# Optimization experiments

Measured on AMD Instinct MI355X. Metric: run time of the kernel, lower is better.

The kernel has to match this reference:

```python
import jax, jax.numpy as jnp
import numpy as np

B, H, W = 32, 256, 256
K = 8          # nonzero voting centers per image
NPIX = 6       # corner pixels per center
MARGIN = 10.0
RATIO_INV = 1e4
LW = {'center': 1.0, 'corner': 1.0, 'corner_offset': 0.25, 'corner_bin_offset': 1.0}


def setup_inputs() -> dict:
    rng = np.random.default_rng(0)
    out0 = rng.standard_normal((B, 7, H, W)).astype(np.float32)
    out1 = rng.standard_normal((B, 7, H, W)).astype(np.float32)
    t_corner = np.zeros((B, 1, H, W), np.float32)
    t_corner_offset = np.zeros((B, 1, 2, H, W), np.float32)
    t_bin = rng.uniform(-0.5, 0.5, (B, 1, 2, H, W)).astype(np.float32)
    anchors = np.zeros((B, K + 1), np.int32)
    positives = np.zeros((B, K + 1), np.int32)
    neg_zero = np.zeros((B, K + 1), np.int32)
    neg_other = np.zeros((B, K), np.int32)
    for b in range(B):
        flat = rng.choice(H * W, size=K * NPIX, replace=False)
        ys, xs = flat // W, flat % W
        t_corner[b, 0, ys, xs] = 1.0
        cvals = rng.choice(np.arange(1, 1000), K, replace=False).astype(np.float32)
        for k in range(K):
            s = slice(k * NPIX, (k + 1) * NPIX)
            v = cvals[k] - (ys[s] + xs[s]).astype(np.float32)
            t_corner_offset[b, 0, 0, ys[s], xs[s]] = 0.5 * v
            t_corner_offset[b, 0, 1, ys[s], xs[s]] = 0.5 * v
        # reproduce the source's voting_map and its random triplet mining
        vm = t_corner_offset[b, 0, 0] + t_corner_offset[b, 0, 1]
        cy, cx = np.nonzero(t_corner[b, 0])
        vm = vm.copy()
        vm[cy, cx] += (cy + cx).astype(np.float32)
        vals = np.unique(vm)  # [0, c1..cK] sorted, zero first
        zero_flat = np.flatnonzero(vm.ravel() == 0)
        nz_flat = np.flatnonzero(vm.ravel() != 0)
        for ci, cv in enumerate(vals):
            idx = np.flatnonzero(vm.ravel() == cv)
            if cv == 0:
                a, p = rng.choice(idx, 2, replace=False)
                anchors[b, ci], positives[b, ci] = a, p
                neg_zero[b, ci] = rng.choice(nz_flat)
            else:
                if len(idx) > 1:
                    a, p = rng.choice(idx, 2, replace=False)
                else:
                    a = p = idx[0]
                anchors[b, ci], positives[b, ci] = a, p
                neg_zero[b, ci] = rng.choice(zero_flat)
                other = np.flatnonzero((vm.ravel() != 0) & (vm.ravel() != cv))
                neg_other[b, ci - 1] = rng.choice(other)
    return {
        'out0': jnp.asarray(out0), 'out1': jnp.asarray(out1),
        't_corner': jnp.asarray(t_corner),
        't_corner_offset': jnp.asarray(t_corner_offset),
        't_bin': jnp.asarray(t_bin),
        'anchors': jnp.asarray(anchors), 'positives': jnp.asarray(positives),
        'neg_zero': jnp.asarray(neg_zero), 'neg_other': jnp.asarray(neg_other),
    }


def _smooth_l1(d):
    ad = jnp.abs(d)
    return jnp.where(ad < 1.0, 0.5 * d * d, ad - 0.5)


def _losses_one_stack(output, t_corner, t_corner_offset, t_bin,
                      anchors, positives, neg_zero, neg_other):
    # output: [B,7,H,W] -> channel-major [7,B,H,W] (matches transpose(0,1).reshape)
    o = jnp.transpose(output, (1, 0, 2, 3))
    center = o[0]                                   # [B,H,W]  (n_jtyp=1)
    corner = o[1:3]                                 # [2,B,H,W]
    scale = jnp.array([H, W], jnp.float32)[:, None, None, None]
    corner_offset = jnp.tanh(o[3:5]) * scale        # [2,B,H,W]
    corner_bin = o[5:7]                             # [2,B,H,W]
    pos = t_corner[:, 0]                            # [B,H,W]

    # --- triplet loss on center predictions (pre-mined indices) ---
    pdf = center.reshape(B, -1)                     # [B,HW]
    va = jnp.take_along_axis(pdf, anchors, 1)       # [B,K+1]
    vp = jnp.take_along_axis(pdf, positives, 1)
    vn1 = jnp.take_along_axis(pdf, neg_zero, 1)
    vn2 = jnp.take_along_axis(pdf, neg_other, 1)    # [B,K]
    Dap = (va - vp) ** 2
    h1 = jax.nn.relu(Dap - (va - vn1) ** 2 + MARGIN)
    h2 = jax.nn.relu(Dap[:, 1:] - (va[:, 1:] - vn2) ** 2 + MARGIN)
    per_center = h1.at[:, 1:].set(0.5 * (h1[:, 1:] + h2))  # nonzero centers avg 2 hinges
    l_center = jnp.mean(jnp.sum(per_center, axis=1) / (K + 1))

    # --- corner cross entropy (ratio-weighted) ---
    nlogp = -jax.nn.log_softmax(corner, axis=0)     # [2,B,H,W]
    l_corner = jnp.mean(pos * nlogp[1] * RATIO_INV + (1.0 - pos) * nlogp[0], axis=(1, 2))

    # --- corner offset smooth-L1 heatmap loss, summed over the 2 coords ---
    tgt = jnp.transpose(t_corner_offset[:, 0], (1, 0, 2, 3))  # [2,B,H,W]
    mask = jnp.where(tgt != 0, RATIO_INV, 1.0)
    l_co = jnp.sum(jnp.mean(mask * _smooth_l1(corner_offset - tgt), axis=(2, 3)), axis=0)

    # --- corner bin offset sigmoid L1 with corner mask, summed over 2 coords ---
    tb = jnp.transpose(t_bin[:, 0], (1, 0, 2, 3))   # [2,B,H,W]
    w = jnp.mean(pos, axis=(1, 2), keepdims=True)   # [B,1,1]
    w = jnp.where(w == 0, 1.0, w)
    lb = jnp.abs(jax.nn.sigmoid(corner_bin) - 0.5 - tb) * (pos / w)[None]
    l_bo = jnp.sum(jnp.mean(lb, axis=(2, 3)), axis=0)

    return jnp.concatenate([
        jnp.array([l_center * LW['center']]),
        l_corner * LW['corner'],
        l_co * LW['corner_offset'],
        l_bo * LW['corner_bin_offset'],
    ])  # [1 + 3B]


def reference(out0, out1, t_corner, t_corner_offset, t_bin,
              anchors, positives, neg_zero, neg_other):
    s0 = _losses_one_stack(out0, t_corner, t_corner_offset, t_bin,
                           anchors, positives, neg_zero, neg_other)
    s1 = _losses_one_stack(out1, t_corner, t_corner_offset, t_bin,
                           anchors, positives, neg_zero, neg_other)
    return jnp.stack([s0, s1])  # [2, 1+3B]
```

## Files before the change

kernel.cpp:

```cpp
#include <hip/hip_runtime.h>

#define BB 32
#define HH 256
#define WW 256
#define HW (HH*WW)
#define HW4 (HW/4)
#define KP1 9
#define KNEG 8
#define MARGIN_F 10.0f
#define RATIO_INV_F 10000.0f


__device__ __forceinline__ float fast_tanh(float x) {
    float xc = fminf(fmaxf(x, -15.f), 15.f);
    float t = __expf(2.f * xc);
    return (t - 1.f) / (t + 1.f);
}
__device__ __forceinline__ float fast_sigmoid(float x) {
    return 1.f / (1.f + __expf(-x));
}
__device__ __forceinline__ float smooth_l1(float d) {
    float ad = fabsf(d);
    return ad < 1.f ? 0.5f * d * d : ad - 0.5f;
}
__device__ __forceinline__ float el(const float4& v, int j) {
    return reinterpret_cast<const float*>(&v)[j];
}

__global__ __launch_bounds__(256) void ml_reduce_kernel(
    const float* __restrict__ out0, const float* __restrict__ out1,
    const float* __restrict__ t_corner, const float* __restrict__ t_co,
    const float* __restrict__ t_bin, float* __restrict__ acc)
{
    const int b = blockIdx.x >> 6;
    const int chunk = blockIdx.x & 63;
    const int i4 = chunk * 256 + threadIdx.x;

    const float4* tc4  = (const float4*)(t_corner + (size_t)b * HW);
    const float4* tco4 = (const float4*)(t_co     + (size_t)b * 2 * HW);
    const float4* tb4  = (const float4*)(t_bin    + (size_t)b * 2 * HW);
    const float4* o04  = (const float4*)(out0 + (size_t)b * 7 * HW);
    const float4* o14  = (const float4*)(out1 + (size_t)b * 7 * HW);

    const float4 pv   = tc4[i4];
    const float4 tg0  = tco4[i4];
    const float4 tg1  = tco4[HW4 + i4];
    const float4 tbv0 = tb4[i4];
    const float4 tbv1 = tb4[HW4 + i4];
    const float4 a0c1 = o04[1 * HW4 + i4];
    const float4 a0c2 = o04[2 * HW4 + i4];
    const float4 a0c3 = o04[3 * HW4 + i4];
    const float4 a0c4 = o04[4 * HW4 + i4];
    const float4 a0c5 = o04[5 * HW4 + i4];
    const float4 a0c6 = o04[6 * HW4 + i4];
    const float4 a1c1 = o14[1 * HW4 + i4];
    const float4 a1c2 = o14[2 * HW4 + i4];
    const float4 a1c3 = o14[3 * HW4 + i4];
    const float4 a1c4 = o14[4 * HW4 + i4];
    const float4 a1c5 = o14[5 * HW4 + i4];
    const float4 a1c6 = o14[6 * HW4 + i4];

    float s_pos = 0.f;
    float s_corner0 = 0.f, s_corner1 = 0.f;
    float s_co0 = 0.f, s_co1 = 0.f;
    float s_bo0 = 0.f, s_bo1 = 0.f;

#pragma unroll
    for (int j = 0; j < 4; ++j) {
        const float pos = el(pv, j);
        s_pos += pos;
        const float tgt0 = el(tg0, j), tgt1 = el(tg1, j);
        const float m0 = (tgt0 != 0.f) ? RATIO_INV_F : 1.f;
        const float m1 = (tgt1 != 0.f) ? RATIO_INV_F : 1.f;
        const float tb0 = el(tbv0, j), tb1 = el(tbv1, j);

        {
            const float c0 = el(a0c1, j), c1 = el(a0c2, j);
            const float mx = fmaxf(c0, c1);
            const float lse = mx + __logf(1.f + __expf(-fabsf(c0 - c1)));
            s_corner0 += pos * (lse - c1) * RATIO_INV_F + (1.f - pos) * (lse - c0);

            const float co0 = fast_tanh(el(a0c3, j)) * (float)HH;
            const float co1 = fast_tanh(el(a0c4, j)) * (float)WW;
            s_co0 += m0 * smooth_l1(co0 - tgt0) + m1 * smooth_l1(co1 - tgt1);

            const float sb0 = fabsf(fast_sigmoid(el(a0c5, j)) - 0.5f - tb0);
            const float sb1 = fabsf(fast_sigmoid(el(a0c6, j)) - 0.5f - tb1);
            s_bo0 += (sb0 + sb1) * pos;
        }
        {
            const float c0 = el(a1c1, j), c1 = el(a1c2, j);
            const float mx = fmaxf(c0, c1);
            const float lse = mx + __logf(1.f + __expf(-fabsf(c0 - c1)));
            s_corner1 += pos * (lse - c1) * RATIO_INV_F + (1.f - pos) * (lse - c0);

            const float co0 = fast_tanh(el(a1c3, j)) * (float)HH;
            const float co1 = fast_tanh(el(a1c4, j)) * (float)WW;
            s_co1 += m0 * smooth_l1(co0 - tgt0) + m1 * smooth_l1(co1 - tgt1);

            const float sb0 = fabsf(fast_sigmoid(el(a1c5, j)) - 0.5f - tb0);
            const float sb1 = fabsf(fast_sigmoid(el(a1c6, j)) - 0.5f - tb1);
            s_bo1 += (sb0 + sb1) * pos;
        }
    }

    __shared__ float part[7][4];
    const int lane = threadIdx.x & 63;
    const int wid  = threadIdx.x >> 6;
    float vals[7] = { s_pos, s_corner0, s_corner1, s_co0, s_co1, s_bo0, s_bo1 };
#pragma unroll
    for (int v = 0; v < 7; ++v) {
        float x = vals[v];
#pragma unroll
        for (int off = 32; off; off >>= 1) x += __shfl_down(x, off);
        if (lane == 0) part[v][wid] = x;
    }
    __syncthreads();
    if (threadIdx.x < 7) {
        const int v = threadIdx.x;
        float x = part[v][0] + part[v][1] + part[v][2] + part[v][3];
        atomicAdd(&acc[v * 32 + b], x);
    }
}

__global__ __launch_bounds__(256) void ml_final_kernel(
    const float* __restrict__ out0, const float* __restrict__ out1,
    const int* __restrict__ anchors, const int* __restrict__ positives,
    const int* __restrict__ neg_zero, const int* __restrict__ neg_other,
    const float* __restrict__ acc, float* __restrict__ out)
{
    __shared__ float lc[2];
    __shared__ float red[2][4];

    float local0 = 0.f, local1 = 0.f;
    for (int i = threadIdx.x; i < 2 * BB * KP1; i += blockDim.x) {
        const int s = i / (BB * KP1);
        const int r = i % (BB * KP1);
        const int b = r / KP1, c = r % KP1;
        const float* o = (s ? out1 : out0) + (size_t)b * 7 * HW;
        const int ia  = anchors  [b * KP1 + c];
        const int ip  = positives[b * KP1 + c];
        const int in1 = neg_zero [b * KP1 + c];
        const float va = o[ia], vp = o[ip], vn1 = o[in1];
        const float Dap = (va - vp) * (va - vp);
        const float h1 = fmaxf(0.f, Dap - (va - vn1) * (va - vn1) + MARGIN_F);
        float pc;
        if (c > 0) {
            const int in2 = neg_other[b * KNEG + (c - 1)];
            const float vn2 = o[in2];
            const float h2 = fmaxf(0.f, Dap - (va - vn2) * (va - vn2) + MARGIN_F);
            pc = 0.5f * (h1 + h2);
        } else {
            pc = h1;
        }
        if (s == 0) local0 += pc; else local1 += pc;
    }

    const int lane = threadIdx.x & 63;
    const int wid  = threadIdx.x >> 6;
    {
        float x = local0;
#pragma unroll
        for (int off = 32; off; off >>= 1) x += __shfl_down(x, off);
        if (lane == 0) red[0][wid] = x;
    }
    {
        float x = local1;
#pragma unroll
        for (int off = 32; off; off >>= 1) x += __shfl_down(x, off);
        if (lane == 0) red[1][wid] = x;
    }
    __syncthreads();
    if (threadIdx.x < 2) {
        lc[threadIdx.x] = (red[threadIdx.x][0] + red[threadIdx.x][1] +
                           red[threadIdx.x][2] + red[threadIdx.x][3]) /
                          (float)(KP1 * BB);
    }
    __syncthreads();

    const float invHW = 1.f / (float)HW;
    for (int i = threadIdx.x; i < 2 * 97; i += blockDim.x) {
        const int s = i / 97, j = i % 97;
        float val;
        if (j == 0) {
            val = lc[s];
        } else if (j < 33) {
            const int b = j - 1;
            val = acc[32 + s * 32 + b] * invHW;
        } else if (j < 65) {
            const int b = j - 33;
            val = 0.25f * acc[96 + s * 32 + b] * invHW;
        } else {
            const int b = j - 65;
            const float sp = acc[b];
            val = (sp > 0.f) ? (acc[160 + s * 32 + b] / sp)
                             : (acc[160 + s * 32 + b] * invHW);
        }
        out[i] = val;
    }
}

extern "C" void kernel_launch(void* const* d_in, const int* in_sizes, int n_in,
                              void* d_out, int out_size, void* d_ws, size_t ws_size,
                              hipStream_t stream) {
    const float* out0      = (const float*)d_in[0];
    const float* out1      = (const float*)d_in[1];
    const float* t_corner  = (const float*)d_in[2];
    const float* t_co      = (const float*)d_in[3];
    const float* t_bin     = (const float*)d_in[4];
    const int*   anchors   = (const int*)d_in[5];
    const int*   positives = (const int*)d_in[6];
    const int*   neg_zero  = (const int*)d_in[7];
    const int*   neg_other = (const int*)d_in[8];
    float* acc = (float*)d_ws;
    float* out = (float*)d_out;

    hipMemsetAsync(acc, 0, 224 * sizeof(float), stream);

    dim3 grid(BB * 64);
    ml_reduce_kernel<<<grid, 256, 0, stream>>>(out0, out1, t_corner, t_co, t_bin, acc);
    ml_final_kernel<<<1, 256, 0, stream>>>(out0, out1, anchors, positives, neg_zero,
                                           neg_other, acc, out);
}
```

Baseline: 191.6 us.

## Split dense reductions and process corner-masked terms sparsely via compacted list

The single fused pass is restructured into a dense kernel and a sparse kernel. The dense kernel computes the unmasked cross-entropy part, the corner offset loss, and a scan of t_corner that builds a list of nonzero corner pixels. The sparse kernel applies the positive-class correction and the bin-offset term only at listed pixels, so t_bin and output channels 5–6 are no longer streamed for every pixel. The cost is an extra launch, a global atomic counter during compaction, and a fixed LIST_CAP that would silently drop entries if more corners existed.

```diff
diff --git a/kernel.cpp b/kernel.cpp
--- a/kernel.cpp
+++ b/kernel.cpp
@@ -9,6 +9,7 @@
 #define KNEG 8
 #define MARGIN_F 10.0f
 #define RATIO_INV_F 10000.0f
+#define LIST_CAP 8192
 
 
 __device__ __forceinline__ float fast_tanh(float x) {
@@ -26,100 +27,121 @@
 __device__ __forceinline__ float el(const float4& v, int j) {
     return reinterpret_cast<const float*>(&v)[j];
 }
-
-__global__ __launch_bounds__(256) void ml_reduce_kernel(
+__device__ __forceinline__ float nlse0(float c0, float c1) {
+    const float mx = fmaxf(c0, c1);
+    return mx + __logf(1.f + __expf(-fabsf(c0 - c1))) - c0;
+}
+
+__device__ __forceinline__ void block_reduce_atomic(float x, float* dst,
+                                                    float* scratch) {
+    const int lane = threadIdx.x & 63;
+    const int wid  = threadIdx.x >> 6;
+#pragma unroll
+    for (int off = 32; off; off >>= 1) x += __shfl_down(x, off);
+    if (lane == 0) scratch[wid] = x;
+    __syncthreads();
+    if (threadIdx.x == 0)
+        atomicAdd(dst, scratch[0] + scratch[1] + scratch[2] + scratch[3]);
+    __syncthreads();
+}
+
+__global__ __launch_bounds__(256) void ml_dense_kernel(
     const float* __restrict__ out0, const float* __restrict__ out1,
     const float* __restrict__ t_corner, const float* __restrict__ t_co,
-    const float* __restrict__ t_bin, float* __restrict__ acc)
+    float* __restrict__ acc, int* __restrict__ wsi)
 {
-    const int b = blockIdx.x >> 6;
-    const int chunk = blockIdx.x & 63;
-    const int i4 = chunk * 256 + threadIdx.x;
-
-    const float4* tc4  = (const float4*)(t_corner + (size_t)b * HW);
-    const float4* tco4 = (const float4*)(t_co     + (size_t)b * 2 * HW);
-    const float4* tb4  = (const float4*)(t_bin    + (size_t)b * 2 * HW);
-    const float4* o04  = (const float4*)(out0 + (size_t)b * 7 * HW);
-    const float4* o14  = (const float4*)(out1 + (size_t)b * 7 * HW);
-
-    const float4 pv   = tc4[i4];
-    const float4 tg0  = tco4[i4];
-    const float4 tg1  = tco4[HW4 + i4];
-    const float4 tbv0 = tb4[i4];
-    const float4 tbv1 = tb4[HW4 + i4];
-    const float4 a0c1 = o04[1 * HW4 + i4];
-    const float4 a0c2 = o04[2 * HW4 + i4];
-    const float4 a0c3 = o04[3 * HW4 + i4];
-    const float4 a0c4 = o04[4 * HW4 + i4];
-    const float4 a0c5 = o04[5 * HW4 + i4];
-    const float4 a0c6 = o04[6 * HW4 + i4];
-    const float4 a1c1 = o14[1 * HW4 + i4];
-    const float4 a1c2 = o14[2 * HW4 + i4];
-    const float4 a1c3 = o14[3 * HW4 + i4];
-    const float4 a1c4 = o14[4 * HW4 + i4];
-    const float4 a1c5 = o14[5 * HW4 + i4];
-    const float4 a1c6 = o14[6 * HW4 + i4];
-
-    float s_pos = 0.f;
-    float s_corner0 = 0.f, s_corner1 = 0.f;
-    float s_co0 = 0.f, s_co1 = 0.f;
-    float s_bo0 = 0.f, s_bo1 = 0.f;
-
-#pragma unroll
-    for (int j = 0; j < 4; ++j) {
-        const float pos = el(pv, j);
-        s_pos += pos;
-        const float tgt0 = el(tg0, j), tgt1 = el(tg1, j);
-        const float m0 = (tgt0 != 0.f) ? RATIO_INV_F : 1.f;
-        const float m1 = (tgt1 != 0.f) ? RATIO_INV_F : 1.f;
-        const float tb0 = el(tbv0, j), tb1 = el(tbv1, j);
-
-        {
-            const float c0 = el(a0c1, j), c1 = el(a0c2, j);
+    __shared__ float scratch[4];
+    const int bid = blockIdx.x;
+
+    if (bid < 4096) {
+        const int s = bid >> 11;
+        const int r = bid & 2047;
+        const int b = r >> 6, chunk = r & 63;
+        const int i4 = chunk * 256 + threadIdx.x;
+        const float* o = (s ? out1 : out0) + (size_t)b * 7 * HW;
+        const float4 v1 = ((const float4*)(o + HW))[i4];
+        const float4 v2 = ((const float4*)(o + 2 * HW))[i4];
+        float sum = 0.f;
+#pragma unroll
+        for (int j = 0; j < 4; ++j) sum += nlse0(el(v1, j), el(v2, j));
+        block_reduce_atomic(sum, &acc[32 + s * 32 + b], scratch);
+    } else if (bid < 6144) {
+        const int r = bid - 4096;
+        const int b = r >> 6, chunk = r & 63;
+        const int i4 = chunk * 256 + threadIdx.x;
+        const float4* tco4 = (const float4*)(t_co + (size_t)b * 2 * HW);
+        const float4* o04  = (const float4*)(out0 + (size_t)b * 7 * HW);
+        const float4* o14  = (const float4*)(out1 + (size_t)b * 7 * HW);
+        const float4 tg0 = tco4[i4];
+        const float4 tg1 = tco4[HW4 + i4];
+        const float4 a03 = o04[3 * HW4 + i4];
+        const float4 a04 = o04[4 * HW4 + i4];
+        const float4 a13 = o14[3 * HW4 + i4];
+        const float4 a14 = o14[4 * HW4 + i4];
+        float s_co0 = 0.f, s_co1 = 0.f;
+#pragma unroll
+        for (int j = 0; j < 4; ++j) {
+            const float tgt0 = el(tg0, j), tgt1 = el(tg1, j);
+            const float m0 = (tgt0 != 0.f) ? RATIO_INV_F : 1.f;
+            const float m1 = (tgt1 != 0.f) ? RATIO_INV_F : 1.f;
+            s_co0 += m0 * smooth_l1(fast_tanh(el(a03, j)) * (float)HH - tgt0)
+                   + m1 * smooth_l1(fast_tanh(el(a04, j)) * (float)WW - tgt1);
+            s_co1 += m0 * smooth_l1(fast_tanh(el(a13, j)) * (float)HH - tgt0)
+                   + m1 * smooth_l1(fast_tanh(el(a14, j)) * (float)WW - tgt1);
+        }
+        block_reduce_atomic(s_co0, &acc[96 + b], scratch);
+        block_reduce_atomic(s_co1, &acc[96 + 32 + b], scratch);
+    } else {
+        const int r = bid - 6144;
+        const int b = r >> 4, c16 = r & 15;
+        const int base4 = c16 * 1024;
+        const float4* tc4 = (const float4*)(t_corner + (size_t)b * HW);
+        float4 v[4];
+#pragma unroll
+        for (int k = 0; k < 4; ++k) v[k] = tc4[base4 + k * 256 + threadIdx.x];
+        float s_pos = 0.f;
+#pragma unroll
+        for (int k = 0; k < 4; ++k) {
+#pragma unroll
+            for (int j = 0; j < 4; ++j) {
+                const float pv = el(v[k], j);
+                if (pv != 0.f) {
+                    s_pos += pv;
+                    const int p = 4 * (base4 + k * 256 + threadIdx.x) + j;
+                    const int idx = atomicAdd(&wsi[224], 1);
+                    if (idx < LIST_CAP) wsi[256 + idx] = (b << 16) | p;
+                }
+            }
+        }
+        block_reduce_atomic(s_pos, &acc[b], scratch);
+    }
+}
+
+__global__ __launch_bounds__(256) void ml_sparse_kernel(
+    const float* __restrict__ out0, const float* __restrict__ out1,
+    const float* __restrict__ t_corner, const float* __restrict__ t_bin,
+    float* __restrict__ acc, const int* __restrict__ wsi)
+{
+    const int n = min(wsi[224], LIST_CAP);
+    for (int i = blockIdx.x * blockDim.x + threadIdx.x; i < n;
+         i += gridDim.x * blockDim.x) {
+        const int e = wsi[256 + i];
+        const int b = e >> 16, p = e & 0xFFFF;
+        const float pos = t_corner[(size_t)b * HW + p];
+        const float tb0 = t_bin[(size_t)b * 2 * HW + p];
+        const float tb1 = t_bin[(size_t)b * 2 * HW + HW + p];
+#pragma unroll
+        for (int s = 0; s < 2; ++s) {
+            const float* o = (s ? out1 : out0) + (size_t)b * 7 * HW;
+            const float c0 = o[HW + p], c1 = o[2 * HW + p];
             const float mx = fmaxf(c0, c1);
             const float lse = mx + __logf(1.f + __expf(-fabsf(c0 - c1)));
-            s_corner0 += pos * (lse - c1) * RATIO_INV_F + (1.f - pos) * (lse - c0);
-
-            const float co0 = fast_tanh(el(a0c3, j)) * (float)HH;
-            const float co1 = fast_tanh(el(a0c4, j)) * (float)WW;
-            s_co0 += m0 * smooth_l1(co0 - tgt0) + m1 * smooth_l1(co1 - tgt1);
-
-            const float sb0 = fabsf(fast_sigmoid(el(a0c5, j)) - 0.5f - tb0);
-            const float sb1 = fabsf(fast_sigmoid(el(a0c6, j)) - 0.5f - tb1);
-            s_bo0 += (sb0 + sb1) * pos;
-        }
-        {
-            const float c0 = el(a1c1, j), c1 = el(a1c2, j);
-            const float mx = fmaxf(c0, c1);
-            const float lse = mx + __logf(1.f + __expf(-fabsf(c0 - c1)));
-            s_corner1 += pos * (lse - c1) * RATIO_INV_F + (1.f - pos) * (lse - c0);
-
-            const float co0 = fast_tanh(el(a1c3, j)) * (float)HH;
-            const float co1 = fast_tanh(el(a1c4, j)) * (float)WW;
-            s_co1 += m0 * smooth_l1(co0 - tgt0) + m1 * smooth_l1(co1 - tgt1);
-
-            const float sb0 = fabsf(fast_sigmoid(el(a1c5, j)) - 0.5f - tb0);
-            const float sb1 = fabsf(fast_sigmoid(el(a1c6, j)) - 0.5f - tb1);
-            s_bo1 += (sb0 + sb1) * pos;
-        }
-    }
-
-    __shared__ float part[7][4];
-    const int lane = threadIdx.x & 63;
-    const int wid  = threadIdx.x >> 6;
-    float vals[7] = { s_pos, s_corner0, s_corner1, s_co0, s_co1, s_bo0, s_bo1 };
-#pragma unroll
-    for (int v = 0; v < 7; ++v) {
-        float x = vals[v];
-#pragma unroll
-        for (int off = 32; off; off >>= 1) x += __shfl_down(x, off);
-        if (lane == 0) part[v][wid] = x;
-    }
-    __syncthreads();
-    if (threadIdx.x < 7) {
-        const int v = threadIdx.x;
-        float x = part[v][0] + part[v][1] + part[v][2] + part[v][3];
-        atomicAdd(&acc[v * 32 + b], x);
+            const float corr = pos * ((lse - c1) * RATIO_INV_F - (lse - c0));
+            atomicAdd(&acc[32 + s * 32 + b], corr);
+            const float sb0 = fabsf(fast_sigmoid(o[5 * HW + p]) - 0.5f - tb0);
+            const float sb1 = fabsf(fast_sigmoid(o[6 * HW + p]) - 0.5f - tb1);
+            atomicAdd(&acc[160 + s * 32 + b], (sb0 + sb1) * pos);
+        }
     }
 }
 
@@ -213,12 +235,13 @@
     const int*   neg_zero  = (const int*)d_in[7];
     const int*   neg_other = (const int*)d_in[8];
     float* acc = (float*)d_ws;
+    int*   wsi = (int*)d_ws;
     float* out = (float*)d_out;
 
-    hipMemsetAsync(acc, 0, 224 * sizeof(float), stream);
-
-    dim3 grid(BB * 64);
-    ml_reduce_kernel<<<grid, 256, 0, stream>>>(out0, out1, t_corner, t_co, t_bin, acc);
+    hipMemsetAsync(d_ws, 0, 1024, stream);
+
+    ml_dense_kernel<<<6656, 256, 0, stream>>>(out0, out1, t_corner, t_co, acc, wsi);
+    ml_sparse_kernel<<<8, 256, 0, stream>>>(out0, out1, t_corner, t_bin, acc, wsi);
     ml_final_kernel<<<1, 256, 0, stream>>>(out0, out1, anchors, positives, neg_zero,
                                            neg_other, acc, out);
 }
```

Result: slower. 199.7 us (+4.3%).
